# Optimization experiments

Hardware: AMD Instinct MI355X
Metric: run time of the kernel (lower is better)

Reference implementation:

```python
import jax, jax.numpy as jnp
import numpy as np

B, NPG, C = 16, 4096, 256          # graphs, nodes per graph per type, feat dim
N = B * NPG                        # nodes per type
E = N * 16                         # edges per edge type (avg degree 16)
RATIO = 0.25
K = int(np.ceil(RATIO * NPG))      # top-k nodes per graph per type


def setup_inputs() -> dict:
    key = jax.random.key(0)
    ks = jax.random.split(key, 16)
    s = 1.0 / np.sqrt(C)
    inp = {
        "x_inst": jax.random.normal(ks[0], (N, C), jnp.float32),
        "x_data": jax.random.normal(ks[1], (N, C), jnp.float32),
        "w_kqv_inst": jax.random.normal(ks[2], (C, 3), jnp.float32) * s,
        "b_kqv_inst": jnp.zeros((3,), jnp.float32),
        "w_kqv_data": jax.random.normal(ks[3], (C, 3), jnp.float32) * s,
        "b_kqv_data": jnp.zeros((3,), jnp.float32),
        "w_out_inst": jax.random.normal(ks[4], (1, 1), jnp.float32),
        "b_out_inst": jnp.zeros((1,), jnp.float32),
        "w_out_data": jax.random.normal(ks[5], (1, 1), jnp.float32),
        "b_out_data": jnp.zeros((1,), jnp.float32),
        "krel_w": jax.random.normal(ks[6], (3,), jnp.float32),
        "krel_b": jnp.zeros((3,), jnp.float32),
        "vrel_w": jax.random.normal(ks[7], (3,), jnp.float32),
        "vrel_b": jnp.zeros((3,), jnp.float32),
        "p_rel": jnp.ones((3,), jnp.float32),
        "ei_i2d": jax.random.randint(ks[8], (2, E), 0, N, jnp.int32),
        "ei_d2i": jax.random.randint(ks[9], (2, E), 0, N, jnp.int32),
        "ei_i2i": jax.random.randint(ks[10], (2, E), 0, N, jnp.int32),
        "batch_inst": jnp.repeat(jnp.arange(B, dtype=jnp.int32), NPG),
        "batch_data": jnp.repeat(jnp.arange(B, dtype=jnp.int32), NPG),
    }
    return inp


def _hgt_scores(x_inst, x_data, w_kqv_inst, b_kqv_inst, w_kqv_data, b_kqv_data,
                w_out_inst, b_out_inst, w_out_data, b_out_data,
                krel_w, krel_b, vrel_w, vrel_b, p_rel,
                ei_i2d, ei_d2i, ei_i2i):
    # HGTConv with out_channels=1, heads=1 -> H=1, D=1 (k,q,v scalar per node)
    kqv_i = x_inst @ w_kqv_inst + b_kqv_inst   # [N,3]
    kqv_d = x_data @ w_kqv_data + b_kqv_data
    k_i, q_i, v_i = kqv_i[:, 0], kqv_i[:, 1], kqv_i[:, 2]
    k_d, q_d, v_d = kqv_d[:, 0], kqv_d[:, 1], kqv_d[:, 2]
    # dst offsets follow node-type order: inst=0, data=N
    q_glob = jnp.concatenate([q_i, q_d])       # [2N]
    Ntot = 2 * N

    def edge_terms(k_src, v_src, ei, t, dst_off):
        s, d = ei[0], ei[1]
        ke = k_src[s] * krel_w[t] + krel_b[t]  # per-relation 1x1 k_rel
        ve = v_src[s] * vrel_w[t] + vrel_b[t]  # per-relation 1x1 v_rel
        dg = d + dst_off
        logit = q_glob[dg] * ke * p_rel[t]     # (q_i*k_j).sum * p_rel / sqrt(D=1)
        return logit, ve, dg

    l0, v0, d0 = edge_terms(k_i, v_i, ei_i2d, 0, N)  # inst->data (dst=data)
    l1, v1, d1 = edge_terms(k_d, v_d, ei_d2i, 1, 0)  # data->inst (dst=inst)
    l2, v2, d2 = edge_terms(k_i, v_i, ei_i2i, 2, 0)  # inst->inst (dst=inst)
    logits = jnp.concatenate([l0, l1, l2])
    vals = jnp.concatenate([v0, v1, v2])
    dst = jnp.concatenate([d0, d1, d2])

    # segment softmax over incoming edges of each destination node
    m = jax.ops.segment_max(logits, dst, num_segments=Ntot)
    m = jnp.where(jnp.isfinite(m), m, 0.0)
    ex = jnp.exp(logits - m[dst])
    den = jax.ops.segment_sum(ex, dst, num_segments=Ntot)
    alpha = ex / den[dst]
    a = jax.ops.segment_sum(alpha * vals, dst, num_segments=Ntot)  # [2N]

    # out_lin (1->1) per node type; skip inactive (1 != 256); GELU (exact)
    s_i = jax.nn.gelu(a[:N, None] * w_out_inst[0, 0] + b_out_inst, approximate=False)
    s_d = jax.nn.gelu(a[N:, None] * w_out_data[0, 0] + b_out_data, approximate=False)
    return s_i, s_d  # [N,1] each


def _pool(x, score):
    # per-graph top-k on score, gate by tanh(score), mean over selected
    sv = score[:, 0].reshape(B, NPG)
    xv = x.reshape(B, NPG, -1)
    topv, topi = jax.lax.top_k(sv, K)                      # [B,K]
    xs = jnp.take_along_axis(xv, topi[:, :, None], axis=1)  # [B,K,C]
    return (xs * jnp.tanh(topv)[:, :, None]).mean(axis=1)   # [B,C]


def reference(x_inst, x_data, w_kqv_inst, b_kqv_inst, w_kqv_data, b_kqv_data,
              w_out_inst, b_out_inst, w_out_data, b_out_data,
              krel_w, krel_b, vrel_w, vrel_b, p_rel,
              ei_i2d, ei_d2i, ei_i2i, batch_inst, batch_data):
    # batch_* are uniform [B x NPG] blocks; pooling uses reshape equivalently.
    s_i, s_d = _hgt_scores(x_inst, x_data, w_kqv_inst, b_kqv_inst,
                           w_kqv_data, b_kqv_data, w_out_inst, b_out_inst,
                           w_out_data, b_out_data, krel_w, krel_b,
                           vrel_w, vrel_b, p_rel, ei_i2d, ei_d2i, ei_i2i)
    return jnp.concatenate([_pool(x_inst, s_i), _pool(x_data, s_d)], axis=-1)  # [B, 2C]
```

## Files before the change

### kernel.cpp

```cpp
#include <hip/hip_runtime.h>
#include <math.h>

constexpr int BB   = 16;
constexpr int NPGc = 4096;
constexpr int Cc   = 256;
constexpr int Nc   = BB * NPGc;
constexpr int Ec   = Nc * 16;
constexpr int Kc   = 1024;
constexpr int NBUK = 512;
constexpr int BUKW = 256;
constexpr int CHUNK = 4096;
constexpr int NCHUNK = (3 * Ec) / CHUNK;

__device__ __forceinline__ unsigned fkey(float f) {
    int b = __float_as_int(f);
    unsigned u = (unsigned)b;
    return (b < 0) ? ~u : (u | 0x80000000u);
}
__device__ __forceinline__ float inv_fkey(unsigned u) {
    unsigned b = (u & 0x80000000u) ? (u ^ 0x80000000u) : ~u;
    return __int_as_float((int)b);
}

__global__ __launch_bounds__(256) void kqv_kernel(
    const float* __restrict__ x_inst, const float* __restrict__ x_data,
    const float* __restrict__ w_inst, const float* __restrict__ b_inst,
    const float* __restrict__ w_data, const float* __restrict__ b_data,
    float2* __restrict__ kv_i, float2* __restrict__ kv_d,
    float* __restrict__ q_glob)
{
    __shared__ float wls[768];
    int tid  = threadIdx.x;
    int wave = tid >> 6, lane = tid & 63;
    int grp  = lane >> 4, l = lane & 15;
    int g    = blockIdx.x * 16 + wave * 4 + grp;
    int row0 = g * 4;
    int side = (row0 >= Nc) ? 1 : 0;
    int node0 = row0 - side * Nc;
    const float* x  = side ? x_data : x_inst;
    const float* w  = side ? w_data : w_inst;
    const float* bp = side ? b_data : b_inst;
    float2* kv = side ? kv_d : kv_i;

    if (tid < 192)
        ((float4*)wls)[tid] = ((const float4*)w)[tid];
    float b0 = bp[0], b1 = bp[1], b2 = bp[2];
    __syncthreads();

    const float4* rp = (const float4*)(x + (size_t)node0 * Cc);
    float4 xv[4][4];
#pragma unroll
    for (int r = 0; r < 4; ++r)
#pragma unroll
        for (int it = 0; it < 4; ++it)
            xv[r][it] = rp[r * 64 + it * 16 + l];

    float kk[4] = {0.f, 0.f, 0.f, 0.f};
    float qq[4] = {0.f, 0.f, 0.f, 0.f};
    float vv[4] = {0.f, 0.f, 0.f, 0.f};
    const float4* wv4 = (const float4*)wls;
#pragma unroll
    for (int it = 0; it < 4; ++it) {
        float4 w0 = wv4[it * 48 + l * 3 + 0];
        float4 w1 = wv4[it * 48 + l * 3 + 1];
        float4 w2 = wv4[it * 48 + l * 3 + 2];
#pragma unroll
        for (int r = 0; r < 4; ++r) {
            float x0 = xv[r][it].x, x1 = xv[r][it].y;
            float x2 = xv[r][it].z, x3 = xv[r][it].w;
            kk[r] = fmaf(x0, w0.x, kk[r]);
            qq[r] = fmaf(x0, w0.y, qq[r]);
            vv[r] = fmaf(x0, w0.z, vv[r]);
            kk[r] = fmaf(x1, w0.w, kk[r]);
            qq[r] = fmaf(x1, w1.x, qq[r]);
            vv[r] = fmaf(x1, w1.y, vv[r]);
            kk[r] = fmaf(x2, w1.z, kk[r]);
            qq[r] = fmaf(x2, w1.w, qq[r]);
            vv[r] = fmaf(x2, w2.x, vv[r]);
            kk[r] = fmaf(x3, w2.y, kk[r]);
            qq[r] = fmaf(x3, w2.z, qq[r]);
            vv[r] = fmaf(x3, w2.w, vv[r]);
        }
    }

#pragma unroll
    for (int r = 0; r < 4; ++r) {
#pragma unroll
        for (int off = 8; off; off >>= 1) {
            kk[r] += __shfl_xor(kk[r], off, 64);
            qq[r] += __shfl_xor(qq[r], off, 64);
            vv[r] += __shfl_xor(vv[r], off, 64);
        }
        if (l == 0) {
            int node = node0 + r;
            kv[node] = make_float2(kk[r] + b0, vv[r] + b2);
            q_glob[side * Nc + node] = qq[r] + b1;
        }
    }
}

__global__ __launch_bounds__(256) void count_kernel(
    const int* __restrict__ ei0, const int* __restrict__ ei1,
    const int* __restrict__ ei2, unsigned* __restrict__ bucket_cnt)
{
    __shared__ unsigned hist[NBUK];
    int tid = threadIdx.x;
    for (int j = tid; j < NBUK; j += 256) hist[j] = 0;
    __syncthreads();
    unsigned base = blockIdx.x * (unsigned)CHUNK;
    int t = (int)(base >> 20);
    unsigned i0 = base & (unsigned)(Ec - 1);
    const int* ei = (t == 0) ? ei0 : (t == 1) ? ei1 : ei2;
    int off = (t == 0) ? Nc : 0;
    const int4* dv = (const int4*)(ei + Ec + i0);
#pragma unroll
    for (int j = 0; j < CHUNK / 1024; ++j) {
        int4 d4 = dv[j * 256 + tid];
        atomicAdd(&hist[(unsigned)(d4.x + off) >> 8], 1u);
        atomicAdd(&hist[(unsigned)(d4.y + off) >> 8], 1u);
        atomicAdd(&hist[(unsigned)(d4.z + off) >> 8], 1u);
        atomicAdd(&hist[(unsigned)(d4.w + off) >> 8], 1u);
    }
    __syncthreads();
    for (int j = tid; j < NBUK; j += 256)
        if (hist[j]) atomicAdd(&bucket_cnt[j], hist[j]);
}

__global__ __launch_bounds__(NBUK) void scan_kernel(
    const unsigned* __restrict__ bucket_cnt,
    unsigned* __restrict__ bucket_base, unsigned* __restrict__ bucket_fill)
{
    __shared__ unsigned s[NBUK];
    int t = threadIdx.x;
    unsigned mine = bucket_cnt[t];
    s[t] = mine;
    __syncthreads();
    for (int off = 1; off < NBUK; off <<= 1) {
        unsigned v = (t >= off) ? s[t - off] : 0u;
        __syncthreads();
        s[t] += v;
        __syncthreads();
    }
    unsigned ex = s[t] - mine;
    bucket_base[t] = ex;
    bucket_fill[t] = ex;
    if (t == NBUK - 1) bucket_base[NBUK] = s[t];
}

__global__ __launch_bounds__(256) void fill_kernel(
    const int* __restrict__ ei0, const int* __restrict__ ei1,
    const int* __restrict__ ei2, unsigned* __restrict__ bucket_fill,
    unsigned* __restrict__ sorted)
{
    __shared__ unsigned hist[NBUK];
    __shared__ unsigned res[NBUK];
    int tid = threadIdx.x;
    for (int j = tid; j < NBUK; j += 256) hist[j] = 0;
    __syncthreads();
    unsigned base = blockIdx.x * (unsigned)CHUNK;
    int t = (int)(base >> 20);
    unsigned i0 = base & (unsigned)(Ec - 1);
    const int* ei = (t == 0) ? ei0 : (t == 1) ? ei1 : ei2;
    int off = (t == 0) ? Nc : 0;
    const int4* dv = (const int4*)(ei + Ec + i0);
    const int4* sv = (const int4*)(ei + i0);
    int4 dreg[CHUNK / 1024];
#pragma unroll
    for (int j = 0; j < CHUNK / 1024; ++j) {
        int4 d4 = dv[j * 256 + tid];
        dreg[j] = d4;
        atomicAdd(&hist[(unsigned)(d4.x + off) >> 8], 1u);
        atomicAdd(&hist[(unsigned)(d4.y + off) >> 8], 1u);
        atomicAdd(&hist[(unsigned)(d4.z + off) >> 8], 1u);
        atomicAdd(&hist[(unsigned)(d4.w + off) >> 8], 1u);
    }
    __syncthreads();
    for (int j = tid; j < NBUK; j += 256) {
        unsigned h = hist[j];
        res[j] = h ? atomicAdd(&bucket_fill[j], h) : 0u;
    }
    __syncthreads();
#pragma unroll
    for (int j = 0; j < CHUNK / 1024; ++j) {
        int4 d4 = dreg[j];
        int4 s4 = sv[j * 256 + tid];
        int dd[4] = {d4.x, d4.y, d4.z, d4.w};
        int ss[4] = {s4.x, s4.y, s4.z, s4.w};
#pragma unroll
        for (int u = 0; u < 4; ++u) {
            int dg  = dd[u] + off;
            int bkt = dg >> 8;
            unsigned pos = atomicAdd(&res[bkt], 1u);
            sorted[pos] =
                (unsigned)ss[u] | ((unsigned)t << 16) | ((unsigned)(dg & 255) << 18);
        }
    }
}

__global__ __launch_bounds__(1024) void bucket_accum_kernel(
    const unsigned* __restrict__ bucket_base, const unsigned* __restrict__ sorted,
    const float* __restrict__ krel_w, const float* __restrict__ krel_b,
    const float* __restrict__ vrel_w, const float* __restrict__ vrel_b,
    const float* __restrict__ p_rel,
    const float2* __restrict__ kv_i, const float2* __restrict__ kv_d,
    const float* __restrict__ q_glob,
    float* __restrict__ den, float* __restrict__ num)
{
    __shared__ float den_l[4 * BUKW];
    __shared__ float num_l[4 * BUKW];
    __shared__ float q_l[BUKW];
    int tid = threadIdx.x;
    int b   = blockIdx.x;
    den_l[tid] = 0.0f; num_l[tid] = 0.0f;
    if (tid < BUKW) q_l[tid] = q_glob[b * BUKW + tid];
    float kw0 = krel_w[0], kw1 = krel_w[1], kw2 = krel_w[2];
    float kb0 = krel_b[0], kb1 = krel_b[1], kb2 = krel_b[2];
    float vw0 = vrel_w[0], vw1 = vrel_w[1], vw2 = vrel_w[2];
    float vb0 = vrel_b[0], vb1 = vrel_b[1], vb2 = vrel_b[2];
    float pr0 = p_rel[0],  pr1 = p_rel[1],  pr2 = p_rel[2];
    unsigned beg = bucket_base[b], end = bucket_base[b + 1];
    int rep = tid & 3;
    __syncthreads();

    for (unsigned e = beg + tid; e < end; e += 1024) {
        unsigned r = sorted[e];
        int s    = (int)(r & 0xFFFFu);
        int t    = (int)((r >> 16) & 3u);
        int low8 = (int)((r >> 18) & 255u);
        float2 kvv = (t == 1) ? kv_d[s] : kv_i[s];
        float kwt = (t == 0) ? kw0 : (t == 1) ? kw1 : kw2;
        float kbt = (t == 0) ? kb0 : (t == 1) ? kb1 : kb2;
        float vwt = (t == 0) ? vw0 : (t == 1) ? vw1 : vw2;
        float vbt = (t == 0) ? vb0 : (t == 1) ? vb1 : vb2;
        float prt = (t == 0) ? pr0 : (t == 1) ? pr1 : pr2;
        float ke = fmaf(kvv.x, kwt, kbt);
        float ve = fmaf(kvv.y, vwt, vbt);
        float logit = q_l[low8] * ke * prt;
        float ex = __expf(fminf(logit, 80.0f));
        int slot = low8 * 4 + rep;
        __hip_atomic_fetch_add(&den_l[slot], ex, __ATOMIC_RELAXED,
                               __HIP_MEMORY_SCOPE_WORKGROUP);
        __hip_atomic_fetch_add(&num_l[slot], ex * ve, __ATOMIC_RELAXED,
                               __HIP_MEMORY_SCOPE_WORKGROUP);
    }
    __syncthreads();
    if (tid < BUKW) {
        den[b * BUKW + tid] = (den_l[tid * 4] + den_l[tid * 4 + 1]) +
                              (den_l[tid * 4 + 2] + den_l[tid * 4 + 3]);
        num[b * BUKW + tid] = (num_l[tid * 4] + num_l[tid * 4 + 1]) +
                              (num_l[tid * 4 + 2] + num_l[tid * 4 + 3]);
    }
}

__global__ __launch_bounds__(1024) void select_kernel(
    const float* __restrict__ den, const float* __restrict__ num,
    const float* __restrict__ w_out_inst, const float* __restrict__ b_out_inst,
    const float* __restrict__ w_out_data, const float* __restrict__ b_out_data,
    int* __restrict__ sel_idx, float* __restrict__ sel_w)
{
    __shared__ unsigned keys[NPGc];
    __shared__ unsigned hist[2048];
    __shared__ unsigned wsum[16];
    __shared__ unsigned short cand[NPGc];
    __shared__ unsigned sh_bin1, sh_rem1, sh_bin2, sh_rem2, sh_cnt, sh_nc;

    int tid  = threadIdx.x;
    int seg  = blockIdx.x;
    int side = seg >> 4;
    int b    = seg & 15;
    float wo = side ? w_out_data[0] : w_out_inst[0];
    float bo = side ? b_out_data[0] : b_out_inst[0];
    int base_node = side * Nc + b * NPGc;
    int base_sel  = seg * Kc;

    unsigned myk[4]; int myj[4];
#pragma unroll
    for (int p = 0; p < 4; ++p) {
        int j = p * 1024 + tid;
        float dn = den[base_node + j];
        float a  = (dn > 0.0f) ? num[base_node + j] / dn : 0.0f;
        float z  = fmaf(a, wo, bo);
        float s  = 0.5f * z * (1.0f + erff(z * 0.70710678f));
        unsigned k32 = fkey(s);
        keys[j] = k32; myk[p] = k32; myj[p] = j;
    }
    if (tid == 0) { sh_cnt = 0; sh_nc = 0; }
    hist[tid] = 0; hist[tid + 1024] = 0;
    __syncthreads();

#pragma unroll
    for (int p = 0; p < 4; ++p) atomicAdd(&hist[myk[p] >> 21], 1u);
    __syncthreads();
    {
        unsigned g0 = hist[2047 - 2 * tid];
        unsigned g1 = hist[2046 - 2 * tid];
        unsigned x = g0 + g1;
        int lane = tid & 63;
#pragma unroll
        for (int off = 1; off < 64; off <<= 1) {
            unsigned y = __shfl_up(x, off, 64);
            if (lane >= off) x += y;
        }
        if (lane == 63) wsum[tid >> 6] = x;
        __syncthreads();
        if (tid < 16) {
            unsigned v = wsum[tid];
#pragma unroll
            for (int off = 1; off < 16; off <<= 1) {
                unsigned y = __shfl_up(v, off, 64);
                if (tid >= off) v += y;
            }
            wsum[tid] = v;
        }
        __syncthreads();
        unsigned basew = (tid >= 64) ? wsum[(tid >> 6) - 1] : 0u;
        unsigned incl  = basew + x;
        unsigned incl0 = incl - g1;
        unsigned K = Kc;
        if (incl0 >= K && incl0 - g0 < K) { sh_bin1 = 2047 - 2 * tid; sh_rem1 = K - (incl0 - g0); }
        if (incl  >= K && incl0     < K) { sh_bin1 = 2046 - 2 * tid; sh_rem1 = K - incl0; }
    }
    __syncthreads();
    unsigned bin1 = sh_bin1, rem1 = sh_rem1;
    hist[tid] = 0; hist[tid + 1024] = 0;
    __syncthreads();

#pragma unroll
    for (int p = 0; p < 4; ++p)
        if ((myk[p] >> 21) == bin1)
            atomicAdd(&hist[(myk[p] >> 10) & 2047u], 1u);
    __syncthreads();
    {
        unsigned g0 = hist[2047 - 2 * tid];
        unsigned g1 = hist[2046 - 2 * tid];
        unsigned x = g0 + g1;
        int lane = tid & 63;
#pragma unroll
        for (int off = 1; off < 64; off <<= 1) {
            unsigned y = __shfl_up(x, off, 64);
            if (lane >= off) x += y;
        }
        if (lane == 63) wsum[tid >> 6] = x;
        __syncthreads();
        if (tid < 16) {
            unsigned v = wsum[tid];
#pragma unroll
            for (int off = 1; off < 16; off <<= 1) {
                unsigned y = __shfl_up(v, off, 64);
                if (tid >= off) v += y;
            }
            wsum[tid] = v;
        }
        __syncthreads();
        unsigned basew = (tid >= 64) ? wsum[(tid >> 6) - 1] : 0u;
        unsigned incl  = basew + x;
        unsigned incl0 = incl - g1;
        unsigned K = rem1;
        if (incl0 >= K && incl0 - g0 < K) { sh_bin2 = 2047 - 2 * tid; sh_rem2 = K - (incl0 - g0); }
        if (incl  >= K && incl0     < K) { sh_bin2 = 2046 - 2 * tid; sh_rem2 = K - incl0; }
    }
    __syncthreads();
    unsigned pref22 = (bin1 << 11) | sh_bin2;
    unsigned rem2 = sh_rem2;

#pragma unroll
    for (int p = 0; p < 4; ++p) {
        unsigned top22 = myk[p] >> 10;
        if (top22 > pref22) {
            unsigned pos = atomicAdd(&sh_cnt, 1u);
            sel_idx[base_sel + pos] = myj[p];
            sel_w[base_sel + pos]   = tanhf(inv_fkey(myk[p]));
        } else if (top22 == pref22) {
            unsigned cp = atomicAdd(&sh_nc, 1u);
            cand[cp] = (unsigned short)myj[p];
        }
    }
    __syncthreads();

    unsigned nc = sh_nc;
    for (unsigned c = tid; c < nc; c += 1024) {
        int j = cand[c];
        unsigned k32 = keys[j];
        unsigned rank = 0;
        for (unsigned q = 0; q < nc; ++q) {
            int jq = cand[q];
            unsigned kq = keys[jq];
            rank += (kq > k32 || (kq == k32 && jq < j)) ? 1u : 0u;
        }
        if (rank < rem2) {
            unsigned pos = atomicAdd(&sh_cnt, 1u);
            sel_idx[base_sel + pos] = j;
            sel_w[base_sel + pos]   = tanhf(inv_fkey(k32));
        }
    }
}

__global__ __launch_bounds__(1024) void pool_kernel(
    const float* __restrict__ x_inst, const float* __restrict__ x_data,
    const int* __restrict__ sel_idx, const float* __restrict__ sel_w,
    float* __restrict__ out)
{
    __shared__ int   ridx[64];
    __shared__ float rw[64];
    __shared__ float accs[256];
    int tid   = threadIdx.x;
    int blk   = blockIdx.x;
    int seg   = blk >> 4;
    int chunk = blk & 15;
    int side  = seg >> 4;
    int b     = seg & 15;
    if (tid < 64) {
        ridx[tid] = sel_idx[seg * Kc + chunk * 64 + tid];
        rw[tid]   = sel_w[seg * Kc + chunk * 64 + tid];
    }
    if (tid < 256) accs[tid] = 0.0f;
    __syncthreads();
    const float* x = side ? x_data : x_inst;
    int w = tid >> 6, l = tid & 63;
    float ax = 0.f, ay = 0.f, az = 0.f, aw = 0.f;
#pragma unroll
    for (int r = 0; r < 4; ++r) {
        int   row = ridx[w * 4 + r];
        float wt  = rw[w * 4 + r];
        float4 xv = ((const float4*)(x + ((size_t)(b * NPGc + row)) * Cc))[l];
        ax = fmaf(xv.x, wt, ax); ay = fmaf(xv.y, wt, ay);
        az = fmaf(xv.z, wt, az); aw = fmaf(xv.w, wt, aw);
    }
    atomicAdd(&accs[l * 4 + 0], ax);
    atomicAdd(&accs[l * 4 + 1], ay);
    atomicAdd(&accs[l * 4 + 2], az);
    atomicAdd(&accs[l * 4 + 3], aw);
    __syncthreads();
    if (tid < 256)
        unsafeAtomicAdd(&out[b * 512 + side * 256 + tid], accs[tid] * (1.0f / (float)Kc));
}

extern "C" void kernel_launch(void* const* d_in, const int* in_sizes, int n_in,
                              void* d_out, int out_size, void* d_ws, size_t ws_size,
                              hipStream_t stream) {
    const float* x_inst     = (const float*)d_in[0];
    const float* x_data     = (const float*)d_in[1];
    const float* w_kqv_inst = (const float*)d_in[2];
    const float* b_kqv_inst = (const float*)d_in[3];
    const float* w_kqv_data = (const float*)d_in[4];
    const float* b_kqv_data = (const float*)d_in[5];
    const float* w_out_inst = (const float*)d_in[6];
    const float* b_out_inst = (const float*)d_in[7];
    const float* w_out_data = (const float*)d_in[8];
    const float* b_out_data = (const float*)d_in[9];
    const float* krel_w     = (const float*)d_in[10];
    const float* krel_b     = (const float*)d_in[11];
    const float* vrel_w     = (const float*)d_in[12];
    const float* vrel_b     = (const float*)d_in[13];
    const float* p_rel      = (const float*)d_in[14];
    const int*   ei_i2d     = (const int*)d_in[15];
    const int*   ei_d2i     = (const int*)d_in[16];
    const int*   ei_i2i     = (const int*)d_in[17];
    float* out = (float*)d_out;

    char* ws = (char*)d_ws;
    float2* kv_i   = (float2*)ws;
    float2* kv_d   = kv_i + Nc;
    float*  q_glob = (float*)(kv_d + Nc);
    float*  den    = q_glob + 2 * Nc;
    float*  num    = den + 2 * Nc;
    unsigned* bucket_cnt  = (unsigned*)(num + 2 * Nc);
    unsigned* bucket_base = bucket_cnt + NBUK;
    unsigned* bucket_fill = bucket_base + NBUK + 1;
    int*      sel_idx     = (int*)(bucket_fill + NBUK);
    float*    sel_w       = (float*)(sel_idx + 32 * Kc);
    unsigned* sorted      = (unsigned*)(sel_w + 32 * Kc);

    hipMemsetAsync(bucket_cnt, 0, NBUK * sizeof(unsigned), stream);
    hipMemsetAsync(d_out, 0, (size_t)out_size * sizeof(float), stream);

    count_kernel<<<NCHUNK, 256, 0, stream>>>(ei_i2d, ei_d2i, ei_i2i, bucket_cnt);
    scan_kernel<<<1, NBUK, 0, stream>>>(bucket_cnt, bucket_base, bucket_fill);
    fill_kernel<<<NCHUNK, 256, 0, stream>>>(ei_i2d, ei_d2i, ei_i2i,
                                            bucket_fill, sorted);

    kqv_kernel<<<(2 * Nc) / 64, 256, 0, stream>>>(
        x_inst, x_data, w_kqv_inst, b_kqv_inst, w_kqv_data, b_kqv_data,
        kv_i, kv_d, q_glob);

    bucket_accum_kernel<<<NBUK, 1024, 0, stream>>>(
        bucket_base, sorted,
        krel_w, krel_b, vrel_w, vrel_b, p_rel,
        kv_i, kv_d, q_glob, den, num);

    select_kernel<<<32, 1024, 0, stream>>>(
        den, num, w_out_inst, b_out_inst, w_out_data, b_out_data,
        sel_idx, sel_w);

    pool_kernel<<<512, 1024, 0, stream>>>(x_inst, x_data, sel_idx, sel_w, out);
}
```

Before: 316.9 us.

## Fuse edge count/scan/fill into one cooperative kernel; retune kqv and accum sizes

Merges the count, scan and fill kernels into a single cooperative-launch kernel that uses two grid-wide syncs. Each block keeps its histogram and destination registers across the phases, so destination indices are read once instead of twice and two kernel launches go away. Separately, it halves rows per thread group in the kqv projection (doubling the grid) and shrinks bucket accumulation blocks from 1024 to 512 threads with 2-way instead of 4-way shared replicas. The cooperative launch needs all 768 blocks co-resident and adds grid-barrier cost, and the smaller accum blocks may raise shared-atomic contention.

```diff
diff --git a/kernel.cpp b/kernel.cpp
--- a/kernel.cpp
+++ b/kernel.cpp
@@ -1,5 +1,8 @@
 #include <hip/hip_runtime.h>
+#include <hip/hip_cooperative_groups.h>
 #include <math.h>
+
+namespace cg = cooperative_groups;
 
 constexpr int BB   = 16;
 constexpr int NPGc = 4096;
@@ -34,7 +37,7 @@
     int wave = tid >> 6, lane = tid & 63;
     int grp  = lane >> 4, l = lane & 15;
     int g    = blockIdx.x * 16 + wave * 4 + grp;
-    int row0 = g * 4;
+    int row0 = g * 2;
     int side = (row0 >= Nc) ? 1 : 0;
     int node0 = row0 - side * Nc;
     const float* x  = side ? x_data : x_inst;
@@ -48,16 +51,16 @@
     __syncthreads();
 
     const float4* rp = (const float4*)(x + (size_t)node0 * Cc);
-    float4 xv[4][4];
-#pragma unroll
-    for (int r = 0; r < 4; ++r)
+    float4 xv[2][4];
+#pragma unroll
+    for (int r = 0; r < 2; ++r)
 #pragma unroll
         for (int it = 0; it < 4; ++it)
             xv[r][it] = rp[r * 64 + it * 16 + l];
 
-    float kk[4] = {0.f, 0.f, 0.f, 0.f};
-    float qq[4] = {0.f, 0.f, 0.f, 0.f};
-    float vv[4] = {0.f, 0.f, 0.f, 0.f};
+    float kk[2] = {0.f, 0.f};
+    float qq[2] = {0.f, 0.f};
+    float vv[2] = {0.f, 0.f};
     const float4* wv4 = (const float4*)wls;
 #pragma unroll
     for (int it = 0; it < 4; ++it) {
@@ -65,7 +68,7 @@
         float4 w1 = wv4[it * 48 + l * 3 + 1];
         float4 w2 = wv4[it * 48 + l * 3 + 2];
 #pragma unroll
-        for (int r = 0; r < 4; ++r) {
+        for (int r = 0; r < 2; ++r) {
             float x0 = xv[r][it].x, x1 = xv[r][it].y;
             float x2 = xv[r][it].z, x3 = xv[r][it].w;
             kk[r] = fmaf(x0, w0.x, kk[r]);
@@ -84,7 +87,7 @@
     }
 
 #pragma unroll
-    for (int r = 0; r < 4; ++r) {
+    for (int r = 0; r < 2; ++r) {
 #pragma unroll
         for (int off = 8; off; off >>= 1) {
             kk[r] += __shfl_xor(kk[r], off, 64);
@@ -99,58 +102,11 @@
     }
 }
 
-__global__ __launch_bounds__(256) void count_kernel(
+__global__ __launch_bounds__(256) void edge_sort_kernel(
     const int* __restrict__ ei0, const int* __restrict__ ei1,
-    const int* __restrict__ ei2, unsigned* __restrict__ bucket_cnt)
-{
-    __shared__ unsigned hist[NBUK];
-    int tid = threadIdx.x;
-    for (int j = tid; j < NBUK; j += 256) hist[j] = 0;
-    __syncthreads();
-    unsigned base = blockIdx.x * (unsigned)CHUNK;
-    int t = (int)(base >> 20);
-    unsigned i0 = base & (unsigned)(Ec - 1);
-    const int* ei = (t == 0) ? ei0 : (t == 1) ? ei1 : ei2;
-    int off = (t == 0) ? Nc : 0;
-    const int4* dv = (const int4*)(ei + Ec + i0);
-#pragma unroll
-    for (int j = 0; j < CHUNK / 1024; ++j) {
-        int4 d4 = dv[j * 256 + tid];
-        atomicAdd(&hist[(unsigned)(d4.x + off) >> 8], 1u);
-        atomicAdd(&hist[(unsigned)(d4.y + off) >> 8], 1u);
-        atomicAdd(&hist[(unsigned)(d4.z + off) >> 8], 1u);
-        atomicAdd(&hist[(unsigned)(d4.w + off) >> 8], 1u);
-    }
-    __syncthreads();
-    for (int j = tid; j < NBUK; j += 256)
-        if (hist[j]) atomicAdd(&bucket_cnt[j], hist[j]);
-}
-
-__global__ __launch_bounds__(NBUK) void scan_kernel(
-    const unsigned* __restrict__ bucket_cnt,
-    unsigned* __restrict__ bucket_base, unsigned* __restrict__ bucket_fill)
-{
-    __shared__ unsigned s[NBUK];
-    int t = threadIdx.x;
-    unsigned mine = bucket_cnt[t];
-    s[t] = mine;
-    __syncthreads();
-    for (int off = 1; off < NBUK; off <<= 1) {
-        unsigned v = (t >= off) ? s[t - off] : 0u;
-        __syncthreads();
-        s[t] += v;
-        __syncthreads();
-    }
-    unsigned ex = s[t] - mine;
-    bucket_base[t] = ex;
-    bucket_fill[t] = ex;
-    if (t == NBUK - 1) bucket_base[NBUK] = s[t];
-}
-
-__global__ __launch_bounds__(256) void fill_kernel(
-    const int* __restrict__ ei0, const int* __restrict__ ei1,
-    const int* __restrict__ ei2, unsigned* __restrict__ bucket_fill,
-    unsigned* __restrict__ sorted)
+    const int* __restrict__ ei2,
+    unsigned* __restrict__ bucket_cnt, unsigned* __restrict__ bucket_base,
+    unsigned* __restrict__ bucket_fill, unsigned* __restrict__ sorted)
 {
     __shared__ unsigned hist[NBUK];
     __shared__ unsigned res[NBUK];
@@ -164,6 +120,7 @@
     int off = (t == 0) ? Nc : 0;
     const int4* dv = (const int4*)(ei + Ec + i0);
     const int4* sv = (const int4*)(ei + i0);
+
     int4 dreg[CHUNK / 1024];
 #pragma unroll
     for (int j = 0; j < CHUNK / 1024; ++j) {
@@ -175,6 +132,39 @@
         atomicAdd(&hist[(unsigned)(d4.w + off) >> 8], 1u);
     }
     __syncthreads();
+    for (int j = tid; j < NBUK; j += 256)
+        if (hist[j]) atomicAdd(&bucket_cnt[j], hist[j]);
+
+    cg::this_grid().sync();
+
+    if (blockIdx.x == 0) {
+        unsigned c0 = __hip_atomic_load(&bucket_cnt[tid], __ATOMIC_RELAXED,
+                                        __HIP_MEMORY_SCOPE_AGENT);
+        unsigned c1 = __hip_atomic_load(&bucket_cnt[tid + 256], __ATOMIC_RELAXED,
+                                        __HIP_MEMORY_SCOPE_AGENT);
+        res[tid] = c0; res[tid + 256] = c1;
+        __syncthreads();
+        for (int offp = 1; offp < NBUK; offp <<= 1) {
+            unsigned v0 = (tid >= offp) ? res[tid - offp] : 0u;
+            unsigned v1 = (tid + 256 >= offp) ? res[tid + 256 - offp] : 0u;
+            __syncthreads();
+            res[tid] += v0; res[tid + 256] += v1;
+            __syncthreads();
+        }
+        unsigned ex0 = res[tid] - c0;
+        unsigned ex1 = res[tid + 256] - c1;
+        bucket_base[tid] = ex0;
+        bucket_base[tid + 256] = ex1;
+        __hip_atomic_store(&bucket_fill[tid], ex0, __ATOMIC_RELAXED,
+                           __HIP_MEMORY_SCOPE_AGENT);
+        __hip_atomic_store(&bucket_fill[tid + 256], ex1, __ATOMIC_RELAXED,
+                           __HIP_MEMORY_SCOPE_AGENT);
+        if (tid == 255) bucket_base[NBUK] = res[NBUK - 1];
+        __syncthreads();
+    }
+
+    cg::this_grid().sync();
+
     for (int j = tid; j < NBUK; j += 256) {
         unsigned h = hist[j];
         res[j] = h ? atomicAdd(&bucket_fill[j], h) : 0u;
@@ -197,7 +187,7 @@
     }
 }
 
-__global__ __launch_bounds__(1024) void bucket_accum_kernel(
+__global__ __launch_bounds__(512) void bucket_accum_kernel(
     const unsigned* __restrict__ bucket_base, const unsigned* __restrict__ sorted,
     const float* __restrict__ krel_w, const float* __restrict__ krel_b,
     const float* __restrict__ vrel_w, const float* __restrict__ vrel_b,
@@ -206,8 +196,8 @@
     const float* __restrict__ q_glob,
     float* __restrict__ den, float* __restrict__ num)
 {
-    __shared__ float den_l[4 * BUKW];
-    __shared__ float num_l[4 * BUKW];
+    __shared__ float den_l[2 * BUKW];
+    __shared__ float num_l[2 * BUKW];
     __shared__ float q_l[BUKW];
     int tid = threadIdx.x;
     int b   = blockIdx.x;
@@ -219,10 +209,10 @@
     float vb0 = vrel_b[0], vb1 = vrel_b[1], vb2 = vrel_b[2];
     float pr0 = p_rel[0],  pr1 = p_rel[1],  pr2 = p_rel[2];
     unsigned beg = bucket_base[b], end = bucket_base[b + 1];
-    int rep = tid & 3;
-    __syncthreads();
-
-    for (unsigned e = beg + tid; e < end; e += 1024) {
+    int rep = tid & 1;
+    __syncthreads();
+
+    for (unsigned e = beg + tid; e < end; e += 512) {
         unsigned r = sorted[e];
         int s    = (int)(r & 0xFFFFu);
         int t    = (int)((r >> 16) & 3u);
@@ -237,7 +227,7 @@
         float ve = fmaf(kvv.y, vwt, vbt);
         float logit = q_l[low8] * ke * prt;
         float ex = __expf(fminf(logit, 80.0f));
-        int slot = low8 * 4 + rep;
+        int slot = low8 * 2 + rep;
         __hip_atomic_fetch_add(&den_l[slot], ex, __ATOMIC_RELAXED,
                                __HIP_MEMORY_SCOPE_WORKGROUP);
         __hip_atomic_fetch_add(&num_l[slot], ex * ve, __ATOMIC_RELAXED,
@@ -245,10 +235,8 @@
     }
     __syncthreads();
     if (tid < BUKW) {
-        den[b * BUKW + tid] = (den_l[tid * 4] + den_l[tid * 4 + 1]) +
-                              (den_l[tid * 4 + 2] + den_l[tid * 4 + 3]);
-        num[b * BUKW + tid] = (num_l[tid * 4] + num_l[tid * 4 + 1]) +
-                              (num_l[tid * 4 + 2] + num_l[tid * 4 + 3]);
+        den[b * BUKW + tid] = den_l[tid * 2] + den_l[tid * 2 + 1];
+        num[b * BUKW + tid] = num_l[tid * 2] + num_l[tid * 2 + 1];
     }
 }
 
@@ -474,16 +462,21 @@
     hipMemsetAsync(bucket_cnt, 0, NBUK * sizeof(unsigned), stream);
     hipMemsetAsync(d_out, 0, (size_t)out_size * sizeof(float), stream);
 
-    count_kernel<<<NCHUNK, 256, 0, stream>>>(ei_i2d, ei_d2i, ei_i2i, bucket_cnt);
-    scan_kernel<<<1, NBUK, 0, stream>>>(bucket_cnt, bucket_base, bucket_fill);
-    fill_kernel<<<NCHUNK, 256, 0, stream>>>(ei_i2d, ei_d2i, ei_i2i,
-                                            bucket_fill, sorted);
-
-    kqv_kernel<<<(2 * Nc) / 64, 256, 0, stream>>>(
+    {
+        void* args[] = {
+            (void*)&ei_i2d, (void*)&ei_d2i, (void*)&ei_i2i,
+            (void*)&bucket_cnt, (void*)&bucket_base, (void*)&bucket_fill,
+            (void*)&sorted
+        };
+        hipLaunchCooperativeKernel((void*)edge_sort_kernel,
+                                   dim3(NCHUNK), dim3(256), args, 0, stream);
+    }
+
+    kqv_kernel<<<(2 * Nc) / 32, 256, 0, stream>>>(
         x_inst, x_data, w_kqv_inst, b_kqv_inst, w_kqv_data, b_kqv_data,
         kv_i, kv_d, q_glob);
 
-    bucket_accum_kernel<<<NBUK, 1024, 0, stream>>>(
+    bucket_accum_kernel<<<NBUK, 512, 0, stream>>>(
         bucket_base, sorted,
         krel_w, krel_b, vrel_w, vrel_b, p_rel,
         kv_i, kv_d, q_glob, den, num);
```

Result: slower. 464.7 us (+46.6%).
